# Kernel optimization log

Measured on AMD Instinct MI355X. Metric: run time of the kernel, lower is better.

The kernel has to match this reference:

```python
import jax, jax.numpy as jnp
import numpy as np

N_NODES = 20000
N_EDGES = 320000
F_IN, HID, OUT = 128, 256, 32
N_LAYERS = 30
N_GRAPHS = 16


def setup_inputs() -> dict:
    key = jax.random.key(0)
    ks = jax.random.split(key, 10)
    x = jax.random.normal(ks[0], (N_NODES, F_IN), dtype=jnp.float32)
    edge_list = jax.random.randint(ks[1], (2, N_EDGES), 0, N_NODES, dtype=jnp.int64)
    batch = jnp.sort(jax.random.randint(ks[2], (N_NODES,), 0, N_GRAPHS, dtype=jnp.int64))
    # GCNConv weights: conv1, 29 middle layers, final linear
    W1 = jax.random.normal(ks[3], (F_IN, HID), dtype=jnp.float32) / np.sqrt(F_IN)
    b1 = jnp.zeros((HID,), dtype=jnp.float32)
    Wm = jax.random.normal(ks[4], (N_LAYERS - 1, HID, HID), dtype=jnp.float32) / np.sqrt(HID)
    bm = jnp.zeros((N_LAYERS - 1, HID), dtype=jnp.float32)
    Wlin = jax.random.normal(ks[5], (HID, OUT), dtype=jnp.float32) / np.sqrt(HID)
    blin = jnp.zeros((OUT,), dtype=jnp.float32)
    return {"x": x, "edge_list": edge_list, "batch": batch,
            "W1": W1, "b1": b1, "Wm": Wm, "bm": bm, "Wlin": Wlin, "blin": blin}


def reference(x, edge_list, batch, W1, b1, Wm, bm, Wlin, blin):
    n = x.shape[0]
    loop = jnp.arange(n, dtype=edge_list.dtype)
    src = jnp.concatenate([edge_list[0], loop])  # senders (+ self loops)
    dst = jnp.concatenate([edge_list[1], loop])  # receivers (+ self loops)
    # symmetric GCN normalization: deg counted at receivers incl. self loops
    deg = jax.ops.segment_sum(jnp.ones_like(dst, dtype=x.dtype), dst, num_segments=n)
    dinv = jnp.where(deg > 0, jax.lax.rsqrt(deg), 0.0)
    norm = dinv[src] * dinv[dst]  # [E+n]

    def conv(h, W, b):
        h = h @ W  # dense linear first (PyG GCNConv)
        agg = jax.ops.segment_sum(h[src] * norm[:, None], dst, num_segments=n)
        return jax.nn.relu(agg + b)

    h = conv(x, W1, b1)

    def step(h, wb):
        W, b = wb
        return conv(h, W, b), None

    h, _ = jax.lax.scan(step, h, (Wm, bm))

    # global mean pool over graphs
    counts = jax.ops.segment_sum(jnp.ones((n,), x.dtype), batch, num_segments=N_GRAPHS)
    pooled = jax.ops.segment_sum(h, batch, num_segments=N_GRAPHS) / jnp.maximum(counts, 1.0)[:, None]
    return pooled @ Wlin + blin
```

## Files before the change

kernel.cpp:

```cpp
#include <hip/hip_runtime.h>

typedef unsigned short u16;
typedef unsigned int u32;
typedef __attribute__((ext_vector_type(8))) _Float16 f16x8;
typedef __attribute__((ext_vector_type(4))) float f32x4;
typedef __attribute__((ext_vector_type(8))) u16 u16x8;

#define N_NODES 20000
#define N_EDGES 320000
#define F_IN 128
#define HID 256
#define OUT_F 32
#define N_LAYERS 30
#define N_GRAPHS 16
#define ELLCAP 64

__device__ __forceinline__ float h2f(u16 u) {
    _Float16 h;
    __builtin_memcpy(&h, &u, 2);
    return (float)h;
}
__device__ __forceinline__ u16 f2h(float f) {
    _Float16 h = (_Float16)f;
    u16 u;
    __builtin_memcpy(&u, &h, 2);
    return u;
}

__device__ __forceinline__ void gl_lds16(const u16* g, u16* l) {
    __builtin_amdgcn_global_load_lds((const u32*)g, (u32*)l, 16, 0, 0);
}

__global__ void fill_ell_kernel(const int* __restrict__ src, const int* __restrict__ dst,
                                int* __restrict__ cursor, u16* __restrict__ ell_col, int E) {
    int e = blockIdx.x * blockDim.x + threadIdx.x;
    if (e >= E) return;
    int s = src[e], d = dst[e];
    int slot = atomicAdd(&cursor[d], 1);
    if (slot < ELLCAP) ell_col[d * ELLCAP + slot] = (u16)s;
}

__global__ void dinv_kernel(const int* __restrict__ cnt, float* __restrict__ dinv, int n) {
    int i = blockIdx.x * blockDim.x + threadIdx.x;
    if (i < n) dinv[i] = rsqrtf((float)(cnt[i] + 1));
}

__global__ void prescale_x_kernel(const float* __restrict__ x, const int* __restrict__ cnt,
                                  u16* __restrict__ xs, int total) {
    int i = blockIdx.x * 256 + threadIdx.x;
    if (i < total) xs[i] = f2h(x[i] * rsqrtf((float)(cnt[i >> 7] + 1)));
}

__global__ __launch_bounds__(256) void transpose_f16_tiled(const float* __restrict__ W,
                                                           u16* __restrict__ T,
                                                           int K, int N) {
    __shared__ float tile[32][33];
    const int l = blockIdx.y;
    const int ntn = N >> 5;
    const int kt = blockIdx.x / ntn, ntile = blockIdx.x % ntn;
    const float* Wl = W + (size_t)l * K * N;
    u16* Tl = T + (size_t)l * K * N;
    const int r8 = threadIdx.x >> 5, c = threadIdx.x & 31;
    #pragma unroll
    for (int rr = 0; rr < 4; ++rr) {
        int r = rr * 8 + r8;
        tile[r][c] = Wl[(size_t)(kt * 32 + r) * N + ntile * 32 + c];
    }
    __syncthreads();
    #pragma unroll
    for (int rr = 0; rr < 4; ++rr) {
        int n = rr * 8 + r8;
        float v = tile[c][n];
        Tl[(size_t)(ntile * 32 + n) * K + kt * 32 + c] = f2h(v);
    }
}

template <int F>
__global__ __launch_bounds__(256) void agg_fsplit_h(const u16* __restrict__ hs,
                                                    const u16* __restrict__ ell_col,
                                                    const int* __restrict__ cnt,
                                                    const float* __restrict__ dinv,
                                                    u16* __restrict__ gout) {
    constexpr int CHUNKS = F / 64;
    __shared__ u16 cols[32 * ELLCAP];
    const int blk = blockIdx.x;
    const int fc = blk & (CHUNKS - 1);
    const int grp = blk / CHUNKS;
    const int node0 = grp * 32;
    const int tid = threadIdx.x;
    *(u16x8*)&cols[tid * 8] = *(const u16x8*)&ell_col[(size_t)node0 * ELLCAP + tid * 8];
    const int g = tid >> 3, sub = tid & 7;
    const int node = node0 + g;
    const int f = fc * 64 + sub * 8;
    int c = cnt[node]; c = c < ELLCAP ? c : ELLCAP;
    const float dd = dinv[node];
    f32x4 acc0 = {}, acc1 = {};
    {
        u16x8 sv = *(const u16x8*)(hs + (size_t)node * F + f);
        #pragma unroll
        for (int i = 0; i < 4; ++i) acc0[i] += h2f(sv[i]);
        #pragma unroll
        for (int i = 0; i < 4; ++i) acc1[i] += h2f(sv[i + 4]);
    }
    __syncthreads();
    const u16* cl = &cols[g * ELLCAP];
    const int nb = (c + 7) >> 3;
    if (nb > 0) {
        u16x8 vbuf[8];
        u16x8 cc = *(const u16x8*)&cl[0];
        #pragma unroll
        for (int j = 0; j < 8; ++j) vbuf[j] = *(const u16x8*)(hs + (size_t)cc[j] * F + f);
        int base = 0;
        for (int b = 1; b < nb; ++b) {
            u16x8 cn = *(const u16x8*)&cl[b * 8];
            u16x8 vn[8];
            #pragma unroll
            for (int j = 0; j < 8; ++j) vn[j] = *(const u16x8*)(hs + (size_t)cn[j] * F + f);
            #pragma unroll
            for (int j = 0; j < 8; ++j) {
                #pragma unroll
                for (int i = 0; i < 4; ++i) acc0[i] += h2f(vbuf[j][i]);
                #pragma unroll
                for (int i = 0; i < 4; ++i) acc1[i] += h2f(vbuf[j][i + 4]);
            }
            base += 8;
            #pragma unroll
            for (int j = 0; j < 8; ++j) vbuf[j] = vn[j];
        }
        const u16x8 zz = {};
        #pragma unroll
        for (int j = 0; j < 8; ++j) {
            u16x8 v = (base + j < c) ? vbuf[j] : zz;
            #pragma unroll
            for (int i = 0; i < 4; ++i) acc0[i] += h2f(v[i]);
            #pragma unroll
            for (int i = 0; i < 4; ++i) acc1[i] += h2f(v[i + 4]);
        }
    }
    u16x8 vh;
    #pragma unroll
    for (int i = 0; i < 4; ++i) vh[i] = f2h(acc0[i] * dd);
    #pragma unroll
    for (int i = 0; i < 4; ++i) vh[i + 4] = f2h(acc1[i] * dd);
    *(u16x8*)(gout + (size_t)node * F + f) = vh;
}

#define NCOLT 4
__global__ __launch_bounds__(256, 4) void gemm_bias_relu(const u16* __restrict__ A,
                                                         const u16* __restrict__ B,
                                                         const float* __restrict__ bias,
                                                         const float* __restrict__ rowscale,
                                                         float* __restrict__ C, u16* __restrict__ Ch,
                                                         int M, int K, int N) {
    __shared__ __align__(16) u16 As[128 * 64];
    __shared__ __align__(16) u16 Bs[64 * 64];
    const int bid = blockIdx.x;
    const int slot = bid & 7;
    const int j = bid >> 3;
    const int ncol = j & (NCOLT - 1);
    const int rowhi = j / NCOLT;
    const int row_tile = rowhi * 8 + slot;
    const int row0 = row_tile * 128;
    if (row0 >= M) return;
    const int n0 = ncol * 64;
    const int tid = threadIdx.x;
    const int wave = tid >> 6, lane = tid & 63;
    const int wm = wave >> 1, wn = wave & 1;
    const int lr = lane >> 3;
    const int lc = lane & 7;
    f32x4 acc[4][2] = {};

    for (int k0 = 0; k0 < K; k0 += 64) {
        #pragma unroll
        for (int q = 0; q < 4; ++q) {
            int rl = (wave * 4 + q) * 8 + lr;
            int ra = row0 + rl; ra = ra < M ? ra : (M - 1);
            int cg = (lc ^ (rl & 7)) << 3;
            gl_lds16(A + (size_t)ra * K + k0 + cg, &As[(wave * 4 + q) * 512]);
        }
        #pragma unroll
        for (int q = 0; q < 2; ++q) {
            int rl = (wave * 2 + q) * 8 + lr;
            int ng = n0 + rl;
            int cg = (lc ^ (rl & 7)) << 3;
            gl_lds16(B + (size_t)ng * K + k0 + cg, &Bs[(wave * 2 + q) * 512]);
        }
        __syncthreads();
        #pragma unroll
        for (int kk = 0; kk < 2; ++kk) {
            const int cidx = kk * 4 + (lane >> 4);
            f16x8 bf[2];
            #pragma unroll
            for (int nt = 0; nt < 2; ++nt) {
                int nl = wn * 32 + nt * 16 + (lane & 15);
                int off = nl * 64 + ((cidx ^ (nl & 7)) << 3);
                bf[nt] = *(const f16x8*)&Bs[off];
            }
            #pragma unroll
            for (int mt = 0; mt < 4; ++mt) {
                int ml = wm * 64 + mt * 16 + (lane & 15);
                int off = ml * 64 + ((cidx ^ (ml & 7)) << 3);
                f16x8 af = *(const f16x8*)&As[off];
                #pragma unroll
                for (int nt = 0; nt < 2; ++nt) {
                    acc[mt][nt] = __builtin_amdgcn_mfma_f32_16x16x32_f16(af, bf[nt], acc[mt][nt], 0, 0, 0);
                }
            }
        }
        __syncthreads();
    }
    #pragma unroll
    for (int mt = 0; mt < 4; ++mt) {
        int gr = row0 + wm * 64 + mt * 16 + ((lane >> 4) << 2);
        #pragma unroll
        for (int r = 0; r < 4; ++r) {
            if (gr + r >= M) continue;
            float sc = rowscale ? rowscale[gr + r] : 1.f;
            #pragma unroll
            for (int nt = 0; nt < 2; ++nt) {
                int gc = n0 + wn * 32 + nt * 16 + (lane & 15);
                float v = sc * fmaxf(acc[mt][nt][r] + bias[gc], 0.f);
                if (Ch) Ch[(size_t)(gr + r) * N + gc] = f2h(v);
                else    C[(size_t)(gr + r) * N + gc] = v;
            }
        }
    }
}

#define POOL_CHUNK 32
__global__ __launch_bounds__(256) void pool_kernel(const float* __restrict__ h,
                                                   const int* __restrict__ batch,
                                                   float* __restrict__ pool_sum) {
    int f = threadIdx.x;
    int start = blockIdx.x * POOL_CHUNK;
    int end = start + POOL_CHUNK; end = end < N_NODES ? end : N_NODES;
    if (start >= N_NODES) return;
    int gcur = batch[start];
    float acc = 0.f;
    for (int i = start; i < end; ++i) {
        int g = batch[i];
        if (g != gcur) { atomicAdd(&pool_sum[gcur * HID + f], acc); acc = 0.f; gcur = g; }
        acc += h[(size_t)i * HID + f];
    }
    atomicAdd(&pool_sum[gcur * HID + f], acc);
}

__device__ int lb_int(const int* __restrict__ a, int n, int v) {
    int lo = 0, hi = n;
    while (lo < hi) {
        int mid = (lo + hi) >> 1;
        if (a[mid] < v) lo = mid + 1; else hi = mid;
    }
    return lo;
}

__global__ void final_linear_kernel(const float* __restrict__ pool_sum,
                                    const int* __restrict__ batch,
                                    const float* __restrict__ Wlin,
                                    const float* __restrict__ blin,
                                    float* __restrict__ out) {
    int idx = blockIdx.x * blockDim.x + threadIdx.x;
    if (idx >= N_GRAPHS * OUT_F) return;
    int g = idx / OUT_F, o = idx % OUT_F;
    int lo = lb_int(batch, N_NODES, g);
    int hi = lb_int(batch, N_NODES, g + 1);
    float cinv = 1.f / fmaxf((float)(hi - lo), 1.f);
    float s = blin[o];
    for (int k = 0; k < HID; ++k) s += (pool_sum[g * HID + k] * cinv) * Wlin[k * OUT_F + o];
    out[idx] = s;
}

static inline size_t align_up(size_t x, size_t a) { return (x + a - 1) & ~(a - 1); }

extern "C" void kernel_launch(void* const* d_in, const int* in_sizes, int n_in,
                              void* d_out, int out_size, void* d_ws, size_t ws_size,
                              hipStream_t stream) {
    const float* x     = (const float*)d_in[0];
    const int*   elist = (const int*)d_in[1];
    const int*   batch = (const int*)d_in[2];
    const float* W1    = (const float*)d_in[3];
    const float* b1    = (const float*)d_in[4];
    const float* Wm    = (const float*)d_in[5];
    const float* bm    = (const float*)d_in[6];
    const float* Wlin  = (const float*)d_in[7];
    const float* blin  = (const float*)d_in[8];
    float* outp = (float*)d_out;

    const int* srcA = elist;
    const int* dstA = elist + N_EDGES;

    char* ws = (char*)d_ws;
    size_t off = 0;
    float* h      = (float*)(ws + off); off = align_up(off + sizeof(float) * N_NODES * HID, 1024);
    u16*   h_half = (u16*)(ws + off);   off = align_up(off + sizeof(u16) * N_NODES * HID, 1024);
    u16*   xs     = (u16*)(ws + off);   off = align_up(off + sizeof(u16) * N_NODES * F_IN, 1024);
    u16*   g_buf  = (u16*)(ws + off);   off = align_up(off + sizeof(u16) * N_NODES * HID, 1024);
    u16*   W1T    = (u16*)(ws + off);   off = align_up(off + sizeof(u16) * F_IN * HID, 1024);
    u16*   WmT    = (u16*)(ws + off);   off = align_up(off + sizeof(u16) * (N_LAYERS - 1) * HID * HID, 1024);
    int*   cursor = (int*)(ws + off);   off = align_up(off + sizeof(int) * N_NODES, 1024);
    float* dinv   = (float*)(ws + off); off = align_up(off + sizeof(float) * N_NODES, 1024);
    u16*   ell_col = (u16*)(ws + off);  off = align_up(off + sizeof(u16) * N_NODES * ELLCAP, 1024);
    float* pool_sum = (float*)(ws + off); off = align_up(off + sizeof(float) * N_GRAPHS * HID, 1024);

    hipMemsetAsync(cursor, 0, sizeof(int) * N_NODES, stream);
    hipMemsetAsync(ell_col, 0, sizeof(u16) * N_NODES * ELLCAP, stream);
    hipMemsetAsync(pool_sum, 0, sizeof(float) * N_GRAPHS * HID, stream);

    fill_ell_kernel<<<(N_EDGES + 255) / 256, 256, 0, stream>>>(srcA, dstA, cursor, ell_col, N_EDGES);
    dinv_kernel<<<(N_NODES + 255) / 256, 256, 0, stream>>>(cursor, dinv, N_NODES);
    prescale_x_kernel<<<(N_NODES * F_IN + 255) / 256, 256, 0, stream>>>(x, cursor, xs, N_NODES * F_IN);

    transpose_f16_tiled<<<dim3((F_IN / 32) * (HID / 32), 1), 256, 0, stream>>>(W1, W1T, F_IN, HID);
    transpose_f16_tiled<<<dim3((HID / 32) * (HID / 32), N_LAYERS - 1), 256, 0, stream>>>(Wm, WmT, HID, HID);

    const int n_row_tiles = (N_NODES + 127) / 128;
    const int ggrid = ((n_row_tiles + 7) / 8) * 8 * NCOLT;
    agg_fsplit_h<F_IN><<<(N_NODES / 32) * (F_IN / 64), 256, 0, stream>>>(xs, ell_col, cursor, dinv, g_buf);
    gemm_bias_relu<<<ggrid, 256, 0, stream>>>(g_buf, W1T, b1, dinv, h, h_half, N_NODES, F_IN, HID);
    for (int l = 0; l < N_LAYERS - 1; ++l) {
        agg_fsplit_h<HID><<<(N_NODES / 32) * (HID / 64), 256, 0, stream>>>(h_half, ell_col, cursor, dinv, g_buf);
        const bool last = (l == N_LAYERS - 2);
        gemm_bias_relu<<<ggrid, 256, 0, stream>>>(g_buf, WmT + (size_t)l * HID * HID,
                                                  bm + (size_t)l * HID,
                                                  last ? nullptr : dinv,
                                                  h, last ? nullptr : h_half,
                                                  N_NODES, HID, HID);
    }
    pool_kernel<<<(N_NODES + POOL_CHUNK - 1) / POOL_CHUNK, 256, 0, stream>>>(h, batch, pool_sum);
    final_linear_kernel<<<2, 256, 0, stream>>>(pool_sum, batch, Wlin, blin, outp);
}
```

Measured before the change: 1.100 ms.

## Fuse neighbor aggregation and GEMM into one per-layer kernel with ping-pong buffers

```diff
diff --git a/kernel.cpp b/kernel.cpp
--- a/kernel.cpp
+++ b/kernel.cpp
@@ -75,153 +75,135 @@
     }
 }
 
-template <int F>
-__global__ __launch_bounds__(256) void agg_fsplit_h(const u16* __restrict__ hs,
-                                                    const u16* __restrict__ ell_col,
-                                                    const int* __restrict__ cnt,
-                                                    const float* __restrict__ dinv,
-                                                    u16* __restrict__ gout) {
-    constexpr int CHUNKS = F / 64;
+template <int K>
+__global__ __launch_bounds__(256, 3) void layer_fused(const u16* __restrict__ hs,
+                                                      const u16* __restrict__ B,
+                                                      const u16* __restrict__ ell_col,
+                                                      const int* __restrict__ cnt,
+                                                      const float* __restrict__ dinv,
+                                                      const float* __restrict__ bias,
+                                                      const float* __restrict__ rowscale,
+                                                      u16* __restrict__ Ch,
+                                                      float* __restrict__ C) {
     __shared__ u16 cols[32 * ELLCAP];
-    const int blk = blockIdx.x;
-    const int fc = blk & (CHUNKS - 1);
-    const int grp = blk / CHUNKS;
-    const int node0 = grp * 32;
+    __shared__ __align__(16) u16 gs[32 * K];
+    __shared__ __align__(16) u16 Bs[256 * 64];
+    const int node0 = blockIdx.x * 32;
     const int tid = threadIdx.x;
     *(u16x8*)&cols[tid * 8] = *(const u16x8*)&ell_col[(size_t)node0 * ELLCAP + tid * 8];
-    const int g = tid >> 3, sub = tid & 7;
-    const int node = node0 + g;
-    const int f = fc * 64 + sub * 8;
+    const int nd = tid >> 3, sub = tid & 7;
+    const int node = node0 + nd;
     int c = cnt[node]; c = c < ELLCAP ? c : ELLCAP;
     const float dd = dinv[node];
-    f32x4 acc0 = {}, acc1 = {};
-    {
-        u16x8 sv = *(const u16x8*)(hs + (size_t)node * F + f);
+    __syncthreads();
+    const u16* cl = &cols[nd * ELLCAP];
+    const int nb = (c + 7) >> 3;
+
+    #pragma unroll 1
+    for (int p = 0; p < K / 64; ++p) {
+        const int f = p * 64 + sub * 8;
+        f32x4 a0 = {}, a1 = {};
+        {
+            u16x8 sv = *(const u16x8*)(hs + (size_t)node * K + f);
+            #pragma unroll
+            for (int i = 0; i < 4; ++i) a0[i] += h2f(sv[i]);
+            #pragma unroll
+            for (int i = 0; i < 4; ++i) a1[i] += h2f(sv[i + 4]);
+        }
+        if (nb > 0) {
+            u16x8 vbuf[8];
+            u16x8 cc = *(const u16x8*)&cl[0];
+            #pragma unroll
+            for (int j = 0; j < 8; ++j) vbuf[j] = *(const u16x8*)(hs + (size_t)cc[j] * K + f);
+            int base = 0;
+            for (int b = 1; b < nb; ++b) {
+                u16x8 cn = *(const u16x8*)&cl[b * 8];
+                u16x8 vn[8];
+                #pragma unroll
+                for (int j = 0; j < 8; ++j) vn[j] = *(const u16x8*)(hs + (size_t)cn[j] * K + f);
+                #pragma unroll
+                for (int j = 0; j < 8; ++j) {
+                    #pragma unroll
+                    for (int i = 0; i < 4; ++i) a0[i] += h2f(vbuf[j][i]);
+                    #pragma unroll
+                    for (int i = 0; i < 4; ++i) a1[i] += h2f(vbuf[j][i + 4]);
+                }
+                base += 8;
+                #pragma unroll
+                for (int j = 0; j < 8; ++j) vbuf[j] = vn[j];
+            }
+            const u16x8 zz = {};
+            #pragma unroll
+            for (int j = 0; j < 8; ++j) {
+                u16x8 v = (base + j < c) ? vbuf[j] : zz;
+                #pragma unroll
+                for (int i = 0; i < 4; ++i) a0[i] += h2f(v[i]);
+                #pragma unroll
+                for (int i = 0; i < 4; ++i) a1[i] += h2f(v[i + 4]);
+            }
+        }
+        u16x8 o;
         #pragma unroll
-        for (int i = 0; i < 4; ++i) acc0[i] += h2f(sv[i]);
+        for (int i = 0; i < 4; ++i) o[i] = f2h(a0[i] * dd);
         #pragma unroll
-        for (int i = 0; i < 4; ++i) acc1[i] += h2f(sv[i + 4]);
-    }
-    __syncthreads();
-    const u16* cl = &cols[g * ELLCAP];
-    const int nb = (c + 7) >> 3;
-    if (nb > 0) {
-        u16x8 vbuf[8];
-        u16x8 cc = *(const u16x8*)&cl[0];
-        #pragma unroll
-        for (int j = 0; j < 8; ++j) vbuf[j] = *(const u16x8*)(hs + (size_t)cc[j] * F + f);
-        int base = 0;
-        for (int b = 1; b < nb; ++b) {
-            u16x8 cn = *(const u16x8*)&cl[b * 8];
-            u16x8 vn[8];
-            #pragma unroll
-            for (int j = 0; j < 8; ++j) vn[j] = *(const u16x8*)(hs + (size_t)cn[j] * F + f);
-            #pragma unroll
-            for (int j = 0; j < 8; ++j) {
-                #pragma unroll
-                for (int i = 0; i < 4; ++i) acc0[i] += h2f(vbuf[j][i]);
-                #pragma unroll
-                for (int i = 0; i < 4; ++i) acc1[i] += h2f(vbuf[j][i + 4]);
-            }
-            base += 8;
-            #pragma unroll
-            for (int j = 0; j < 8; ++j) vbuf[j] = vn[j];
-        }
-        const u16x8 zz = {};
-        #pragma unroll
-        for (int j = 0; j < 8; ++j) {
-            u16x8 v = (base + j < c) ? vbuf[j] : zz;
-            #pragma unroll
-            for (int i = 0; i < 4; ++i) acc0[i] += h2f(v[i]);
-            #pragma unroll
-            for (int i = 0; i < 4; ++i) acc1[i] += h2f(v[i + 4]);
-        }
-    }
-    u16x8 vh;
-    #pragma unroll
-    for (int i = 0; i < 4; ++i) vh[i] = f2h(acc0[i] * dd);
-    #pragma unroll
-    for (int i = 0; i < 4; ++i) vh[i + 4] = f2h(acc1[i] * dd);
-    *(u16x8*)(gout + (size_t)node * F + f) = vh;
-}
-
-#define NCOLT 4
-__global__ __launch_bounds__(256, 4) void gemm_bias_relu(const u16* __restrict__ A,
-                                                         const u16* __restrict__ B,
-                                                         const float* __restrict__ bias,
-                                                         const float* __restrict__ rowscale,
-                                                         float* __restrict__ C, u16* __restrict__ Ch,
-                                                         int M, int K, int N) {
-    __shared__ __align__(16) u16 As[128 * 64];
-    __shared__ __align__(16) u16 Bs[64 * 64];
-    const int bid = blockIdx.x;
-    const int slot = bid & 7;
-    const int j = bid >> 3;
-    const int ncol = j & (NCOLT - 1);
-    const int rowhi = j / NCOLT;
-    const int row_tile = rowhi * 8 + slot;
-    const int row0 = row_tile * 128;
-    if (row0 >= M) return;
-    const int n0 = ncol * 64;
-    const int tid = threadIdx.x;
+        for (int i = 0; i < 4; ++i) o[i + 4] = f2h(a1[i] * dd);
+        const int cc_ = p * 8 + sub;
+        *(u16x8*)&gs[nd * K + ((cc_ ^ (nd & 7)) << 3)] = o;
+    }
+
     const int wave = tid >> 6, lane = tid & 63;
-    const int wm = wave >> 1, wn = wave & 1;
-    const int lr = lane >> 3;
-    const int lc = lane & 7;
-    f32x4 acc[4][2] = {};
-
-    for (int k0 = 0; k0 < K; k0 += 64) {
-        #pragma unroll
-        for (int q = 0; q < 4; ++q) {
-            int rl = (wave * 4 + q) * 8 + lr;
-            int ra = row0 + rl; ra = ra < M ? ra : (M - 1);
-            int cg = (lc ^ (rl & 7)) << 3;
-            gl_lds16(A + (size_t)ra * K + k0 + cg, &As[(wave * 4 + q) * 512]);
-        }
-        #pragma unroll
-        for (int q = 0; q < 2; ++q) {
-            int rl = (wave * 2 + q) * 8 + lr;
-            int ng = n0 + rl;
-            int cg = (lc ^ (rl & 7)) << 3;
-            gl_lds16(B + (size_t)ng * K + k0 + cg, &Bs[(wave * 2 + q) * 512]);
-        }
+    const int lr = lane >> 3, lc = lane & 7;
+    #pragma unroll
+    for (int q = 0; q < 8; ++q) {
+        int rl = (wave * 8 + q) * 8 + lr;
+        gl_lds16(B + (size_t)rl * K + ((lc ^ (rl & 7)) << 3), &Bs[(wave * 8 + q) * 512]);
+    }
+    f32x4 acc[2][4] = {};
+    #pragma unroll
+    for (int k = 0; k < K / 64; ++k) {
         __syncthreads();
+        const int k0 = k * 64;
         #pragma unroll
         for (int kk = 0; kk < 2; ++kk) {
-            const int cidx = kk * 4 + (lane >> 4);
-            f16x8 bf[2];
-            #pragma unroll
-            for (int nt = 0; nt < 2; ++nt) {
-                int nl = wn * 32 + nt * 16 + (lane & 15);
-                int off = nl * 64 + ((cidx ^ (nl & 7)) << 3);
-                bf[nt] = *(const f16x8*)&Bs[off];
-            }
-            #pragma unroll
-            for (int mt = 0; mt < 4; ++mt) {
-                int ml = wm * 64 + mt * 16 + (lane & 15);
-                int off = ml * 64 + ((cidx ^ (ml & 7)) << 3);
-                f16x8 af = *(const f16x8*)&As[off];
-                #pragma unroll
-                for (int nt = 0; nt < 2; ++nt) {
+            const int c8 = kk * 4 + (lane >> 4);
+            f16x8 bf[4];
+            #pragma unroll
+            for (int nt = 0; nt < 4; ++nt) {
+                int n = wave * 64 + nt * 16 + (lane & 15);
+                bf[nt] = *(const f16x8*)&Bs[n * 64 + ((c8 ^ (n & 7)) << 3)];
+            }
+            #pragma unroll
+            for (int mt = 0; mt < 2; ++mt) {
+                int ml = mt * 16 + (lane & 15);
+                int cg = (k0 >> 3) + c8;
+                f16x8 af = *(const f16x8*)&gs[ml * K + ((cg ^ (ml & 7)) << 3)];
+                #pragma unroll
+                for (int nt = 0; nt < 4; ++nt)
                     acc[mt][nt] = __builtin_amdgcn_mfma_f32_16x16x32_f16(af, bf[nt], acc[mt][nt], 0, 0, 0);
-                }
-            }
-        }
-        __syncthreads();
-    }
-    #pragma unroll
-    for (int mt = 0; mt < 4; ++mt) {
-        int gr = row0 + wm * 64 + mt * 16 + ((lane >> 4) << 2);
+            }
+        }
+        if (k + 1 < K / 64) {
+            __syncthreads();
+            const int kn = k0 + 64;
+            #pragma unroll
+            for (int q = 0; q < 8; ++q) {
+                int rl = (wave * 8 + q) * 8 + lr;
+                gl_lds16(B + (size_t)rl * K + kn + ((lc ^ (rl & 7)) << 3), &Bs[(wave * 8 + q) * 512]);
+            }
+        }
+    }
+    #pragma unroll
+    for (int mt = 0; mt < 2; ++mt) {
+        int gr = node0 + mt * 16 + ((lane >> 4) << 2);
         #pragma unroll
         for (int r = 0; r < 4; ++r) {
-            if (gr + r >= M) continue;
             float sc = rowscale ? rowscale[gr + r] : 1.f;
             #pragma unroll
-            for (int nt = 0; nt < 2; ++nt) {
-                int gc = n0 + wn * 32 + nt * 16 + (lane & 15);
+            for (int nt = 0; nt < 4; ++nt) {
+                int gc = wave * 64 + nt * 16 + (lane & 15);
                 float v = sc * fmaxf(acc[mt][nt][r] + bias[gc], 0.f);
-                if (Ch) Ch[(size_t)(gr + r) * N + gc] = f2h(v);
-                else    C[(size_t)(gr + r) * N + gc] = v;
+                if (Ch) Ch[(size_t)(gr + r) * HID + gc] = f2h(v);
+                else    C[(size_t)(gr + r) * HID + gc] = v;
             }
         }
     }
@@ -292,9 +274,9 @@
     char* ws = (char*)d_ws;
     size_t off = 0;
     float* h      = (float*)(ws + off); off = align_up(off + sizeof(float) * N_NODES * HID, 1024);
-    u16*   h_half = (u16*)(ws + off);   off = align_up(off + sizeof(u16) * N_NODES * HID, 1024);
+    u16*   hA     = (u16*)(ws + off);   off = align_up(off + sizeof(u16) * N_NODES * HID, 1024);
+    u16*   hB     = (u16*)(ws + off);   off = align_up(off + sizeof(u16) * N_NODES * HID, 1024);
     u16*   xs     = (u16*)(ws + off);   off = align_up(off + sizeof(u16) * N_NODES * F_IN, 1024);
-    u16*   g_buf  = (u16*)(ws + off);   off = align_up(off + sizeof(u16) * N_NODES * HID, 1024);
     u16*   W1T    = (u16*)(ws + off);   off = align_up(off + sizeof(u16) * F_IN * HID, 1024);
     u16*   WmT    = (u16*)(ws + off);   off = align_up(off + sizeof(u16) * (N_LAYERS - 1) * HID * HID, 1024);
     int*   cursor = (int*)(ws + off);   off = align_up(off + sizeof(int) * N_NODES, 1024);
@@ -313,18 +295,17 @@
     transpose_f16_tiled<<<dim3((F_IN / 32) * (HID / 32), 1), 256, 0, stream>>>(W1, W1T, F_IN, HID);
     transpose_f16_tiled<<<dim3((HID / 32) * (HID / 32), N_LAYERS - 1), 256, 0, stream>>>(Wm, WmT, HID, HID);
 
-    const int n_row_tiles = (N_NODES + 127) / 128;
-    const int ggrid = ((n_row_tiles + 7) / 8) * 8 * NCOLT;
-    agg_fsplit_h<F_IN><<<(N_NODES / 32) * (F_IN / 64), 256, 0, stream>>>(xs, ell_col, cursor, dinv, g_buf);
-    gemm_bias_relu<<<ggrid, 256, 0, stream>>>(g_buf, W1T, b1, dinv, h, h_half, N_NODES, F_IN, HID);
+    const int lgrid = N_NODES / 32;
+    layer_fused<F_IN><<<lgrid, 256, 0, stream>>>(xs, W1T, ell_col, cursor, dinv, b1, dinv, hA, h);
+    u16* cur = hA; u16* nxt = hB;
     for (int l = 0; l < N_LAYERS - 1; ++l) {
-        agg_fsplit_h<HID><<<(N_NODES / 32) * (HID / 64), 256, 0, stream>>>(h_half, ell_col, cursor, dinv, g_buf);
         const bool last = (l == N_LAYERS - 2);
-        gemm_bias_relu<<<ggrid, 256, 0, stream>>>(g_buf, WmT + (size_t)l * HID * HID,
-                                                  bm + (size_t)l * HID,
-                                                  last ? nullptr : dinv,
-                                                  h, last ? nullptr : h_half,
-                                                  N_NODES, HID, HID);
+        layer_fused<HID><<<lgrid, 256, 0, stream>>>(cur, WmT + (size_t)l * HID * HID,
+                                                    ell_col, cursor, dinv,
+                                                    bm + (size_t)l * HID,
+                                                    last ? nullptr : dinv,
+                                                    last ? nullptr : nxt, h);
+        u16* t = cur; cur = nxt; nxt = t;
     }
     pool_kernel<<<(N_NODES + POOL_CHUNK - 1) / POOL_CHUNK, 256, 0, stream>>>(h, batch, pool_sum);
     final_linear_kernel<<<2, 256, 0, stream>>>(pool_sum, batch, Wlin, blin, outp);
```

Result: faster. 930.9 us (-15.3%).
